# Optimization experiments

Hardware: AMD Instinct MI355X
Metric: run time of the kernel (lower is better)

Reference implementation:

```python
import jax, jax.numpy as jnp
import numpy as np

K = 2  # top-k experts per token


def setup_inputs() -> dict:
    key = jax.random.key(0)
    k1, k2, k3, k4 = jax.random.split(key, 4)
    B, S, D, E = 4, 4096, 1024, 64
    x = jax.random.normal(k1, (B, S, D), dtype=jnp.float32)
    gate_w = jax.random.normal(k2, (E, D), dtype=jnp.float32) * (1.0 / np.sqrt(D))
    noise_weight = jax.random.normal(k3, (E,), dtype=jnp.float32) * 0.02
    noise = jax.random.normal(k4, (B, S, E), dtype=jnp.float32)  # randn_like(logits) * noisy_std(=1.0)
    return {"x": x, "gate_w": gate_w, "noise_weight": noise_weight, "noise": noise}


def reference(x, gate_w, noise_weight, noise):
    E = gate_w.shape[0]
    # logits = x @ W^T  -> [B, S, E]
    logits = jnp.einsum("bsd,ed->bse", x, gate_w)
    logits_noisy = logits + noise * noise_weight  # noisy_std = 1.0 folded into `noise`
    top_vals, top_idx = jax.lax.top_k(logits_noisy, K)  # [B,S,K]
    # scatter top-k logits into a -inf mask, then softmax over experts
    keep = jax.nn.one_hot(top_idx, E, dtype=jnp.bool_).any(axis=-2)  # [B,S,E]
    neg_inf = jnp.finfo(logits_noisy.dtype).min
    sparse = jnp.where(keep, logits_noisy, neg_inf)
    weights = jax.nn.softmax(sparse, axis=-1)
    return weights, top_idx
```

## Files before the change

kernel.cpp:

```cpp
#include <hip/hip_runtime.h>
#include <math.h>


#define DDIM 1024
#define NEXP 64
#define NTOK 16384
#define NSPLIT 8
#define CPB 2

typedef float f4 __attribute__((ext_vector_type(4)));
typedef short s8 __attribute__((ext_vector_type(8)));
typedef unsigned int u32;

static __device__ __forceinline__ void split3(float f, short& h, short& m, short& l) {
    const u32 uf = __float_as_uint(f);
    h = (short)(uf >> 16);
    const float r1 = f - __uint_as_float(uf & 0xffff0000u);
    const u32 u1 = __float_as_uint(r1);
    m = (short)(u1 >> 16);
    const float r2 = r1 - __uint_as_float(u1 & 0xffff0000u);
    l = (short)(__float_as_uint(r2) >> 16);
}

__global__ __launch_bounds__(256)
void w_prep(const float* __restrict__ gw, short* __restrict__ wimg) {
    const int uid = blockIdx.x * 256 + threadIdx.x;
    const int c   = uid >> 9;
    const int kk  = (uid >> 8) & 1;
    const int e   = (uid >> 2) & 63;
    const int q   = uid & 3;
    const int k0  = c * 64 + kk * 32 + q * 8;
    const float* src = gw + (size_t)e * DDIM + k0;
    s8 hv, mv, lv;
    #pragma unroll
    for (int j = 0; j < 8; ++j) {
        short h, m, l;
        split3(src[j], h, m, l);
        hv[j] = h; mv[j] = m; lv[j] = l;
    }
    const size_t base = (size_t)c * 1536 + (kk * 3) * 256
                      + (e >> 4) * 64 + q * 16 + (e & 15);
    *(s8*)(wimg + (base      ) * 8) = hv;
    *(s8*)(wimg + (base + 256) * 8) = mv;
    *(s8*)(wimg + (base + 512) * 8) = lv;
}

__global__ __launch_bounds__(256, 4)
void gemm_partial(const float* __restrict__ x,
                  const short* __restrict__ wimg,
                  float* __restrict__ part)
{
    const int tid   = threadIdx.x;
    const int lane  = tid & 63;
    const int wv    = tid >> 6;
    const int m     = lane & 15;
    const int q     = lane >> 4;
    const int tile  = blockIdx.x & 255;
    const int split = blockIdx.x >> 8;
    const int tokBase = tile * 64 + wv * 16;

    const float* xrow = x + (size_t)(tokBase + m) * DDIM
                      + split * (CPB * 64) + q * 8;

    f4 acc0[4], acc1[4];
    #pragma unroll
    for (int t = 0; t < 4; ++t) { acc0[t] = (f4)0.f; acc1[t] = (f4)0.f; }

    f4 stage[2][4];
    stage[0][0] = *(const f4*)(xrow);
    stage[0][1] = *(const f4*)(xrow + 4);
    stage[0][2] = *(const f4*)(xrow + 32);
    stage[0][3] = *(const f4*)(xrow + 36);

    #pragma unroll
    for (int cc = 0; cc < CPB; ++cc) {
        if (cc + 1 < CPB) {
            const float* s = xrow + (cc + 1) * 64;
            stage[(cc + 1) & 1][0] = *(const f4*)(s);
            stage[(cc + 1) & 1][1] = *(const f4*)(s + 4);
            stage[(cc + 1) & 1][2] = *(const f4*)(s + 32);
            stage[(cc + 1) & 1][3] = *(const f4*)(s + 36);
        }

        s8 ah[2], am[2], al[2];
        const float* sv = (const float*)stage[cc & 1];
        #pragma unroll
        for (int kk = 0; kk < 2; ++kk)
            #pragma unroll
            for (int j = 0; j < 8; ++j) {
                short h, mm, l;
                split3(sv[kk * 8 + j], h, mm, l);
                ah[kk][j] = h; am[kk][j] = mm; al[kk][j] = l;
            }

        const short* cb = wimg + (size_t)(split * CPB + cc) * (1536 * 8);
        #pragma unroll
        for (int kk = 0; kk < 2; ++kk) {
            #pragma unroll
            for (int t = 0; t < 4; ++t) {
                const int pb = (kk * 3) * 256 + t * 64 + lane;
                const s8 bh = *(const s8*)(cb + (size_t)(pb      ) * 8);
                const s8 bm = *(const s8*)(cb + (size_t)(pb + 256) * 8);
                const s8 bl = *(const s8*)(cb + (size_t)(pb + 512) * 8);
                acc0[t] = __builtin_amdgcn_mfma_f32_16x16x32_bf16(ah[kk], bh, acc0[t], 0, 0, 0);
                acc1[t] = __builtin_amdgcn_mfma_f32_16x16x32_bf16(ah[kk], bm, acc1[t], 0, 0, 0);
                acc1[t] = __builtin_amdgcn_mfma_f32_16x16x32_bf16(am[kk], bh, acc1[t], 0, 0, 0);
                acc1[t] = __builtin_amdgcn_mfma_f32_16x16x32_bf16(ah[kk], bl, acc1[t], 0, 0, 0);
                acc1[t] = __builtin_amdgcn_mfma_f32_16x16x32_bf16(am[kk], bm, acc1[t], 0, 0, 0);
                acc1[t] = __builtin_amdgcn_mfma_f32_16x16x32_bf16(al[kk], bh, acc1[t], 0, 0, 0);
            }
        }
    }

    #pragma unroll
    for (int t = 0; t < 4; ++t)
        #pragma unroll
        for (int r = 0; r < 4; ++r)
            part[((size_t)split * NTOK + tokBase + q * 4 + r) * NEXP + m + 16 * t]
                = acc0[t][r] + acc1[t][r];
}

__global__ __launch_bounds__(256)
void reduce_topk(const float* __restrict__ part,
                 const float* __restrict__ noise_weight,
                 const float* __restrict__ noise,
                 float* __restrict__ out_w,
                 float* __restrict__ out_i)
{
    const int lane  = threadIdx.x & 63;
    const int wv    = threadIdx.x >> 6;
    const int token = blockIdx.x * 4 + wv;

    float sum = 0.f;
    #pragma unroll
    for (int s = 0; s < NSPLIT; ++s)
        sum += part[((size_t)s * NTOK + token) * NEXP + lane];

    const float ln = fmaf(noise[(size_t)token * NEXP + lane], noise_weight[lane], sum);

    float v1 = ln; int i1 = lane;
    #pragma unroll
    for (int off = 32; off > 0; off >>= 1) {
        const float vo = __shfl_xor(v1, off, 64);
        const int   io = __shfl_xor(i1, off, 64);
        if (vo > v1 || (vo == v1 && io < i1)) { v1 = vo; i1 = io; }
    }
    float v2 = (lane == i1) ? -3.4e38f : ln; int i2 = lane;
    #pragma unroll
    for (int off = 32; off > 0; off >>= 1) {
        const float vo = __shfl_xor(v2, off, 64);
        const int   io = __shfl_xor(i2, off, 64);
        if (vo > v2 || (vo == v2 && io < i2)) { v2 = vo; i2 = io; }
    }

    const float d   = expf(v2 - v1);
    const float inv = 1.f / (1.f + d);
    const float wgt = (lane == i1) ? inv : ((lane == i2) ? d * inv : 0.f);
    out_w[(size_t)token * NEXP + lane] = wgt;
    if (lane == 0) {
        out_i[(size_t)token * 2]     = (float)i1;
        out_i[(size_t)token * 2 + 1] = (float)i2;
    }
}

extern "C" void kernel_launch(void* const* d_in, const int* in_sizes, int n_in,
                              void* d_out, int out_size, void* d_ws, size_t ws_size,
                              hipStream_t stream) {
    const float* x     = (const float*)d_in[0];
    const float* gw    = (const float*)d_in[1];
    const float* nwt   = (const float*)d_in[2];
    const float* noise = (const float*)d_in[3];
    float* out_w = (float*)d_out;
    float* out_i = (float*)d_out + (size_t)NTOK * NEXP;

    short* wimg = (short*)d_ws;
    float* part = (float*)((char*)d_ws + 512 * 1024);

    hipLaunchKernelGGL(w_prep, dim3(32), dim3(256), 0, stream, gw, wimg);
    hipLaunchKernelGGL(gemm_partial, dim3(256 * NSPLIT), dim3(256), 0, stream,
                       x, wimg, part);
    hipLaunchKernelGGL(reduce_topk, dim3(NTOK / 4), dim3(256), 0, stream,
                       part, nwt, noise, out_w, out_i);
}
```

Before: 134.4 us.

## Stage weight image in LDS via async global_load_lds and preload all x chunks

Each block now copies its split's pre-split bf16 weight image (48KB) into shared memory with direct global-to-LDS loads. All four waves then read B fragments from LDS instead of each wave fetching them separately from global memory. All A (x) loads for both chunks are issued up front rather than double-buffered. Occupancy hint drops from 4 to 3 blocks per CU because of the larger LDS footprint, and a block-wide barrier is added before compute.

```diff
diff --git a/kernel.cpp b/kernel.cpp
--- a/kernel.cpp
+++ b/kernel.cpp
@@ -7,6 +7,7 @@
 #define NTOK 16384
 #define NSPLIT 8
 #define CPB 2
+#define CHUNK_SH 12288
 
 typedef float f4 __attribute__((ext_vector_type(4)));
 typedef short s8 __attribute__((ext_vector_type(8)));
@@ -20,6 +21,12 @@
     m = (short)(u1 >> 16);
     const float r2 = r1 - __uint_as_float(u1 & 0xffff0000u);
     l = (short)(__float_as_uint(r2) >> 16);
+}
+
+static __device__ __forceinline__ void gl_lds16(const void* g, void* l) {
+    __builtin_amdgcn_global_load_lds(
+        (const __attribute__((address_space(1))) u32*)g,
+        (__attribute__((address_space(3))) u32*)l, 16, 0, 0);
 }
 
 __global__ __launch_bounds__(256)
@@ -45,11 +52,13 @@
     *(s8*)(wimg + (base + 512) * 8) = lv;
 }
 
-__global__ __launch_bounds__(256, 4)
+__global__ __launch_bounds__(256, 3)
 void gemm_partial(const float* __restrict__ x,
                   const short* __restrict__ wimg,
                   float* __restrict__ part)
 {
+    __shared__ short bs[CPB * CHUNK_SH];
+
     const int tid   = threadIdx.x;
     const int lane  = tid & 63;
     const int wv    = tid >> 6;
@@ -59,31 +68,34 @@
     const int split = blockIdx.x >> 8;
     const int tokBase = tile * 64 + wv * 16;
 
+    const short* bsrc = wimg + (size_t)(split * CPB) * CHUNK_SH;
+    #pragma unroll
+    for (int i = 0; i < 12; ++i) {
+        const int off = (wv * 12 + i) * 512;
+        gl_lds16(bsrc + off + lane * 8, &bs[off]);
+    }
+
     const float* xrow = x + (size_t)(tokBase + m) * DDIM
                       + split * (CPB * 64) + q * 8;
+    f4 A[8];
+    #pragma unroll
+    for (int cc = 0; cc < CPB; ++cc) {
+        A[cc * 4 + 0] = *(const f4*)(xrow + cc * 64);
+        A[cc * 4 + 1] = *(const f4*)(xrow + cc * 64 + 4);
+        A[cc * 4 + 2] = *(const f4*)(xrow + cc * 64 + 32);
+        A[cc * 4 + 3] = *(const f4*)(xrow + cc * 64 + 36);
+    }
 
     f4 acc0[4], acc1[4];
     #pragma unroll
     for (int t = 0; t < 4; ++t) { acc0[t] = (f4)0.f; acc1[t] = (f4)0.f; }
 
-    f4 stage[2][4];
-    stage[0][0] = *(const f4*)(xrow);
-    stage[0][1] = *(const f4*)(xrow + 4);
-    stage[0][2] = *(const f4*)(xrow + 32);
-    stage[0][3] = *(const f4*)(xrow + 36);
+    __syncthreads();
 
     #pragma unroll
     for (int cc = 0; cc < CPB; ++cc) {
-        if (cc + 1 < CPB) {
-            const float* s = xrow + (cc + 1) * 64;
-            stage[(cc + 1) & 1][0] = *(const f4*)(s);
-            stage[(cc + 1) & 1][1] = *(const f4*)(s + 4);
-            stage[(cc + 1) & 1][2] = *(const f4*)(s + 32);
-            stage[(cc + 1) & 1][3] = *(const f4*)(s + 36);
-        }
-
         s8 ah[2], am[2], al[2];
-        const float* sv = (const float*)stage[cc & 1];
+        const float* sv = (const float*)&A[cc * 4];
         #pragma unroll
         for (int kk = 0; kk < 2; ++kk)
             #pragma unroll
@@ -93,15 +105,14 @@
                 ah[kk][j] = h; am[kk][j] = mm; al[kk][j] = l;
             }
 
-        const short* cb = wimg + (size_t)(split * CPB + cc) * (1536 * 8);
         #pragma unroll
         for (int kk = 0; kk < 2; ++kk) {
             #pragma unroll
             for (int t = 0; t < 4; ++t) {
-                const int pb = (kk * 3) * 256 + t * 64 + lane;
-                const s8 bh = *(const s8*)(cb + (size_t)(pb      ) * 8);
-                const s8 bm = *(const s8*)(cb + (size_t)(pb + 256) * 8);
-                const s8 bl = *(const s8*)(cb + (size_t)(pb + 512) * 8);
+                const int pb = cc * 1536 + (kk * 3) * 256 + t * 64 + lane;
+                const s8 bh = *(const s8*)&bs[(size_t)(pb      ) * 8];
+                const s8 bm = *(const s8*)&bs[(size_t)(pb + 256) * 8];
+                const s8 bl = *(const s8*)&bs[(size_t)(pb + 512) * 8];
                 acc0[t] = __builtin_amdgcn_mfma_f32_16x16x32_bf16(ah[kk], bh, acc0[t], 0, 0, 0);
                 acc1[t] = __builtin_amdgcn_mfma_f32_16x16x32_bf16(ah[kk], bm, acc1[t], 0, 0, 0);
                 acc1[t] = __builtin_amdgcn_mfma_f32_16x16x32_bf16(am[kk], bh, acc1[t], 0, 0, 0);
```

New measurement: 124.9 us. 1.08x faster.

## Fuse GEMM split-K reduction and top-k softmax into one kernel via LDS

Applied to the files above, without the earlier changes.

Replaces the two-kernel scheme (global split-K partial sums, then a reduce/top-k kernel) with one kernel. Each block handles 16 tokens, and its four waves each cover a quarter of the K dimension. Partial results are reduced in shared memory before the top-k and softmax run in the same block. This removes the 32MB partials round trip to global memory and one launch. The cost is fewer tokens per block, lower occupancy (launch bounds 3), and each block re-reading the whole weight image. B-fragment loads are also batched ahead of the MFMAs.

```diff
diff --git a/kernel.cpp b/kernel.cpp
--- a/kernel.cpp
+++ b/kernel.cpp
@@ -5,8 +5,8 @@
 #define DDIM 1024
 #define NEXP 64
 #define NTOK 16384
-#define NSPLIT 8
-#define CPB 2
+#define CPW 4
+#define CHUNK_SH 12288
 
 typedef float f4 __attribute__((ext_vector_type(4)));
 typedef short s8 __attribute__((ext_vector_type(8)));
@@ -45,45 +45,45 @@
     *(s8*)(wimg + (base + 512) * 8) = lv;
 }
 
-__global__ __launch_bounds__(256, 4)
-void gemm_partial(const float* __restrict__ x,
-                  const short* __restrict__ wimg,
-                  float* __restrict__ part)
+static __device__ __forceinline__ bool bt(float av, int ai, float bv, int bi) {
+    return av > bv || (av == bv && ai < bi);
+}
+
+__global__ __launch_bounds__(256, 3)
+void moe_fused(const float* __restrict__ x,
+               const short* __restrict__ wimg,
+               const float* __restrict__ nwt,
+               const float* __restrict__ noise,
+               float* __restrict__ out_w,
+               float* __restrict__ out_i)
 {
-    const int tid   = threadIdx.x;
-    const int lane  = tid & 63;
-    const int wv    = tid >> 6;
-    const int m     = lane & 15;
-    const int q     = lane >> 4;
-    const int tile  = blockIdx.x & 255;
-    const int split = blockIdx.x >> 8;
-    const int tokBase = tile * 64 + wv * 16;
+    __shared__ float red[4][16][NEXP];
 
-    const float* xrow = x + (size_t)(tokBase + m) * DDIM
-                      + split * (CPB * 64) + q * 8;
+    const int tid  = threadIdx.x;
+    const int lane = tid & 63;
+    const int wv   = tid >> 6;
+    const int m    = lane & 15;
+    const int q    = lane >> 4;
+    const int tokBase = blockIdx.x * 16;
+
+    const float* xrow = x + (size_t)(tokBase + m) * DDIM + wv * (CPW * 64) + q * 8;
 
     f4 acc0[4], acc1[4];
     #pragma unroll
     for (int t = 0; t < 4; ++t) { acc0[t] = (f4)0.f; acc1[t] = (f4)0.f; }
 
-    f4 stage[2][4];
-    stage[0][0] = *(const f4*)(xrow);
-    stage[0][1] = *(const f4*)(xrow + 4);
-    stage[0][2] = *(const f4*)(xrow + 32);
-    stage[0][3] = *(const f4*)(xrow + 36);
+    f4 As[4];
+    As[0] = *(const f4*)(xrow);
+    As[1] = *(const f4*)(xrow + 4);
+    As[2] = *(const f4*)(xrow + 32);
+    As[3] = *(const f4*)(xrow + 36);
 
     #pragma unroll
-    for (int cc = 0; cc < CPB; ++cc) {
-        if (cc + 1 < CPB) {
-            const float* s = xrow + (cc + 1) * 64;
-            stage[(cc + 1) & 1][0] = *(const f4*)(s);
-            stage[(cc + 1) & 1][1] = *(const f4*)(s + 4);
-            stage[(cc + 1) & 1][2] = *(const f4*)(s + 32);
-            stage[(cc + 1) & 1][3] = *(const f4*)(s + 36);
-        }
+    for (int cc = 0; cc < CPW; ++cc) {
+        const short* cb = wimg + (size_t)(wv * CPW + cc) * CHUNK_SH;
 
         s8 ah[2], am[2], al[2];
-        const float* sv = (const float*)stage[cc & 1];
+        const float* sv = (const float*)&As[0];
         #pragma unroll
         for (int kk = 0; kk < 2; ++kk)
             #pragma unroll
@@ -93,21 +93,32 @@
                 ah[kk][j] = h; am[kk][j] = mm; al[kk][j] = l;
             }
 
-        const short* cb = wimg + (size_t)(split * CPB + cc) * (1536 * 8);
+        if (cc + 1 < CPW) {
+            const float* s = xrow + (cc + 1) * 64;
+            As[0] = *(const f4*)(s);
+            As[1] = *(const f4*)(s + 4);
+            As[2] = *(const f4*)(s + 32);
+            As[3] = *(const f4*)(s + 36);
+        }
+
         #pragma unroll
         for (int kk = 0; kk < 2; ++kk) {
+            s8 bh[4], bm[4], bl[4];
             #pragma unroll
             for (int t = 0; t < 4; ++t) {
                 const int pb = (kk * 3) * 256 + t * 64 + lane;
-                const s8 bh = *(const s8*)(cb + (size_t)(pb      ) * 8);
-                const s8 bm = *(const s8*)(cb + (size_t)(pb + 256) * 8);
-                const s8 bl = *(const s8*)(cb + (size_t)(pb + 512) * 8);
-                acc0[t] = __builtin_amdgcn_mfma_f32_16x16x32_bf16(ah[kk], bh, acc0[t], 0, 0, 0);
-                acc1[t] = __builtin_amdgcn_mfma_f32_16x16x32_bf16(ah[kk], bm, acc1[t], 0, 0, 0);
-                acc1[t] = __builtin_amdgcn_mfma_f32_16x16x32_bf16(am[kk], bh, acc1[t], 0, 0, 0);
-                acc1[t] = __builtin_amdgcn_mfma_f32_16x16x32_bf16(ah[kk], bl, acc1[t], 0, 0, 0);
-                acc1[t] = __builtin_amdgcn_mfma_f32_16x16x32_bf16(am[kk], bm, acc1[t], 0, 0, 0);
-                acc1[t] = __builtin_amdgcn_mfma_f32_16x16x32_bf16(al[kk], bh, acc1[t], 0, 0, 0);
+                bh[t] = *(const s8*)(cb + (size_t)(pb      ) * 8);
+                bm[t] = *(const s8*)(cb + (size_t)(pb + 256) * 8);
+                bl[t] = *(const s8*)(cb + (size_t)(pb + 512) * 8);
+            }
+            #pragma unroll
+            for (int t = 0; t < 4; ++t) {
+                acc0[t] = __builtin_amdgcn_mfma_f32_16x16x32_bf16(ah[kk], bh[t], acc0[t], 0, 0, 0);
+                acc1[t] = __builtin_amdgcn_mfma_f32_16x16x32_bf16(ah[kk], bm[t], acc1[t], 0, 0, 0);
+                acc1[t] = __builtin_amdgcn_mfma_f32_16x16x32_bf16(am[kk], bh[t], acc1[t], 0, 0, 0);
+                acc1[t] = __builtin_amdgcn_mfma_f32_16x16x32_bf16(ah[kk], bl[t], acc1[t], 0, 0, 0);
+                acc1[t] = __builtin_amdgcn_mfma_f32_16x16x32_bf16(am[kk], bm[t], acc1[t], 0, 0, 0);
+                acc1[t] = __builtin_amdgcn_mfma_f32_16x16x32_bf16(al[kk], bh[t], acc1[t], 0, 0, 0);
             }
         }
     }
@@ -116,50 +127,42 @@
     for (int t = 0; t < 4; ++t)
         #pragma unroll
         for (int r = 0; r < 4; ++r)
-            part[((size_t)split * NTOK + tokBase + q * 4 + r) * NEXP + m + 16 * t]
-                = acc0[t][r] + acc1[t][r];
-}
+            red[wv][q * 4 + r][m + 16 * t] = acc0[t][r] + acc1[t][r];
 
-__global__ __launch_bounds__(256)
-void reduce_topk(const float* __restrict__ part,
-                 const float* __restrict__ noise_weight,
-                 const float* __restrict__ noise,
-                 float* __restrict__ out_w,
-                 float* __restrict__ out_i)
-{
-    const int lane  = threadIdx.x & 63;
-    const int wv    = threadIdx.x >> 6;
-    const int token = blockIdx.x * 4 + wv;
+    __syncthreads();
 
-    float sum = 0.f;
+    const float nw = nwt[lane];
     #pragma unroll
-    for (int s = 0; s < NSPLIT; ++s)
-        sum += part[((size_t)s * NTOK + token) * NEXP + lane];
+    for (int r = 0; r < 4; ++r) {
+        const int lt  = wv * 4 + r;
+        const int tok = tokBase + lt;
+        const float sum = (red[0][lt][lane] + red[1][lt][lane])
+                        + (red[2][lt][lane] + red[3][lt][lane]);
+        const float ln = fmaf(noise[(size_t)tok * NEXP + lane], nw, sum);
 
-    const float ln = fmaf(noise[(size_t)token * NEXP + lane], noise_weight[lane], sum);
+        float v1 = ln; int i1 = lane;
+        #pragma unroll
+        for (int off = 32; off > 0; off >>= 1) {
+            const float vo = __shfl_xor(v1, off, 64);
+            const int   io = __shfl_xor(i1, off, 64);
+            if (bt(vo, io, v1, i1)) { v1 = vo; i1 = io; }
+        }
+        float v2 = (lane == i1) ? -3.4e38f : ln; int i2 = lane;
+        #pragma unroll
+        for (int off = 32; off > 0; off >>= 1) {
+            const float vo = __shfl_xor(v2, off, 64);
+            const int   io = __shfl_xor(i2, off, 64);
+            if (bt(vo, io, v2, i2)) { v2 = vo; i2 = io; }
+        }
 
-    float v1 = ln; int i1 = lane;
-    #pragma unroll
-    for (int off = 32; off > 0; off >>= 1) {
-        const float vo = __shfl_xor(v1, off, 64);
-        const int   io = __shfl_xor(i1, off, 64);
-        if (vo > v1 || (vo == v1 && io < i1)) { v1 = vo; i1 = io; }
-    }
-    float v2 = (lane == i1) ? -3.4e38f : ln; int i2 = lane;
-    #pragma unroll
-    for (int off = 32; off > 0; off >>= 1) {
-        const float vo = __shfl_xor(v2, off, 64);
-        const int   io = __shfl_xor(i2, off, 64);
-        if (vo > v2 || (vo == v2 && io < i2)) { v2 = vo; i2 = io; }
-    }
-
-    const float d   = expf(v2 - v1);
-    const float inv = 1.f / (1.f + d);
-    const float wgt = (lane == i1) ? inv : ((lane == i2) ? d * inv : 0.f);
-    out_w[(size_t)token * NEXP + lane] = wgt;
-    if (lane == 0) {
-        out_i[(size_t)token * 2]     = (float)i1;
-        out_i[(size_t)token * 2 + 1] = (float)i2;
+        const float d   = expf(v2 - v1);
+        const float inv = 1.f / (1.f + d);
+        const float wgt = (lane == i1) ? inv : ((lane == i2) ? d * inv : 0.f);
+        out_w[(size_t)tok * NEXP + lane] = wgt;
+        if (lane == 0) {
+            out_i[(size_t)tok * 2]     = (float)i1;
+            out_i[(size_t)tok * 2 + 1] = (float)i2;
+        }
     }
 }
 
@@ -172,13 +175,9 @@
     const float* noise = (const float*)d_in[3];
     float* out_w = (float*)d_out;
     float* out_i = (float*)d_out + (size_t)NTOK * NEXP;
-
-    short* wimg = (short*)d_ws;
-    float* part = (float*)((char*)d_ws + 512 * 1024);
+    short* wimg  = (short*)d_ws;
 
     hipLaunchKernelGGL(w_prep, dim3(32), dim3(256), 0, stream, gw, wimg);
-    hipLaunchKernelGGL(gemm_partial, dim3(256 * NSPLIT), dim3(256), 0, stream,
-                       x, wimg, part);
-    hipLaunchKernelGGL(reduce_topk, dim3(NTOK / 4), dim3(256), 0, stream,
-                       part, nwt, noise, out_w, out_i);
+    hipLaunchKernelGGL(moe_fused, dim3(NTOK / 16), dim3(256), 0, stream,
+                       x, wimg, nwt, noise, out_w, out_i);
 }
```

Measured after the change: 125.1 us. -6.9%, faster.
